# Performance work log

Measured on AMD Instinct MI355X. Metric: run time of the kernel, lower is better.

The kernel has to match this reference:

```python
import jax, jax.numpy as jnp
import numpy as np

B, S, D, H = 2, 2048, 1024, 16
HD = D // H
SCALE = HD ** -0.5

def setup_inputs() -> dict:
    key = jax.random.key(0)
    ks = jax.random.split(key, 5)
    x = jax.random.normal(ks[0], (B, S, D), dtype=jnp.float32)
    Wqkv = jax.random.normal(ks[1], (D, 3 * D), dtype=jnp.float32) * (D ** -0.5)
    bqkv = jnp.zeros((3 * D,), dtype=jnp.float32)
    Wproj = jax.random.normal(ks[2], (D, D), dtype=jnp.float32) * (D ** -0.5)
    bproj = jnp.zeros((D,), dtype=jnp.float32)
    return {"x": x, "Wqkv": Wqkv, "bqkv": bqkv, "Wproj": Wproj, "bproj": bproj}

def reference(x, Wqkv, bqkv, Wproj, bproj):
    b, s, _ = x.shape
    qkv = x @ Wqkv + bqkv                       # [B,S,3D]
    qkv = qkv.reshape(b, s, 3, H, HD)
    q, k, v = [jnp.transpose(qkv[:, :, i], (0, 2, 1, 3)) for i in range(3)]  # [B,H,S,HD]
    attn = jnp.einsum('bhqd,bhkd->bhqk', q, k) * SCALE   # [B,H,S,S]
    attn = jax.nn.softmax(attn, axis=-1)
    out = jnp.einsum('bhqk,bhkd->bhqd', attn, v)         # [B,H,S,HD]
    out = jnp.transpose(out, (0, 2, 1, 3)).reshape(b, s, D)
    return out @ Wproj + bproj
```

## Files before the change

### kernel.cpp

```cpp
#include <hip/hip_runtime.h>
#include <hip/hip_bf16.h>

#define BB 2
#define SS 2048
#define DD 1024
#define HH 16
#define HDD 64
#define MM (BB*SS)
#define NQKV (3*DD)
#define SCALE 0.125f
#define QPRESCALE 0.18033688f

typedef __bf16 bf16_t;
typedef bf16_t bf16x4 __attribute__((ext_vector_type(4)));
typedef bf16_t bf16x8 __attribute__((ext_vector_type(8)));
typedef float f32x4 __attribute__((ext_vector_type(4)));
typedef float f32x16 __attribute__((ext_vector_type(16)));

__device__ __forceinline__ void gl_lds16(const bf16_t* g, bf16_t* l) {
    __builtin_amdgcn_global_load_lds(
        (const __attribute__((address_space(1))) unsigned int*)(uintptr_t)g,
        (__attribute__((address_space(3))) unsigned int*)(uintptr_t)l,
        16, 0, 0);
}

__global__ __launch_bounds__(256) void convert_f32_bf16(
    const float* __restrict__ src, bf16_t* __restrict__ dst, int n)
{
    int i = (blockIdx.x * 256 + threadIdx.x) * 8;
    if (i < n) {
        float4 a = *(const float4*)(src + i);
        float4 b = *(const float4*)(src + i + 4);
        bf16x8 v;
        v[0]=(bf16_t)a.x; v[1]=(bf16_t)a.y; v[2]=(bf16_t)a.z; v[3]=(bf16_t)a.w;
        v[4]=(bf16_t)b.x; v[5]=(bf16_t)b.y; v[6]=(bf16_t)b.z; v[7]=(bf16_t)b.w;
        *reinterpret_cast<bf16x8*>(dst + i) = v;
    }
}

__global__ __launch_bounds__(256) void transpose2_f32_bf16(
    const float* __restrict__ Wqkv, const float* __restrict__ Wproj,
    bf16_t* __restrict__ wqkvt, bf16_t* __restrict__ wprojt)
{
    __shared__ float tile[32][33];
    const int bx = blockIdx.x;
    const float* src; bf16_t* dst; int C, bxl;
    if (bx < 96) { src = Wqkv;  dst = wqkvt;  C = NQKV; bxl = bx; }
    else         { src = Wproj; dst = wprojt; C = DD;   bxl = bx - 96; }
    const int R = DD;
    const int tx = threadIdx.x & 31, ty = threadIdx.x >> 5;
    const int r0 = blockIdx.y * 32, c0 = bxl * 32;
    #pragma unroll
    for (int i = 0; i < 32; i += 8)
        tile[ty + i][tx] = src[(size_t)(r0 + ty + i) * C + c0 + tx];
    __syncthreads();
    #pragma unroll
    for (int i = 0; i < 32; i += 8)
        dst[(size_t)(c0 + ty + i) * R + r0 + tx] = (bf16_t)tile[tx][ty + i];
}

template <int MODE>
__global__ __launch_bounds__(256) void gemm_bt(
    const bf16_t* __restrict__ A, const bf16_t* __restrict__ Bt,
    const float* __restrict__ bias, float* __restrict__ outf,
    bf16_t* __restrict__ qw, bf16_t* __restrict__ kw, bf16_t* __restrict__ vtw,
    int N, int K)
{
    __shared__ __align__(16) bf16_t As[128 * 32];
    __shared__ __align__(16) bf16_t Bs[128 * 32];

    const int tid  = threadIdx.x;
    const int w    = tid >> 6;
    const int lane = tid & 63;
    const int lr   = lane & 15;
    const int quad = lane >> 4;
    const int m0   = blockIdx.y * 128;
    const int n0   = blockIdx.x * 128;
    const int wm   = w >> 1;
    const int wn   = w & 1;

    f32x4 acc[4][4];
    #pragma unroll
    for (int i = 0; i < 4; i++)
        #pragma unroll
        for (int j = 0; j < 4; j++) acc[i][j] = (f32x4){0.f, 0.f, 0.f, 0.f};

    const int stgRow = lane >> 2;
    const int stgCol = (lane & 3) * 8;
    const bf16_t* aPtr = A  + (size_t)(m0 + w * 32 + stgRow) * K + stgCol;
    const bf16_t* bPtr = Bt + (size_t)(n0 + w * 32 + stgRow) * K + stgCol;
    bf16_t* aDst = As + w * 1024;
    bf16_t* bDst = Bs + w * 1024;
    const size_t rowSkip = (size_t)16 * K;

    for (int ks = 0; ks < K; ks += 32) {
        __syncthreads();
        gl_lds16(aPtr + ks,           aDst);
        gl_lds16(aPtr + rowSkip + ks, aDst + 512);
        gl_lds16(bPtr + ks,           bDst);
        gl_lds16(bPtr + rowSkip + ks, bDst + 512);
        __syncthreads();

        bf16x8 af[4], bf[4];
        #pragma unroll
        for (int mi = 0; mi < 4; mi++)
            af[mi] = *reinterpret_cast<const bf16x8*>(&As[(wm * 64 + mi * 16 + lr) * 32 + quad * 8]);
        #pragma unroll
        for (int ni = 0; ni < 4; ni++)
            bf[ni] = *reinterpret_cast<const bf16x8*>(&Bs[(wn * 64 + ni * 16 + lr) * 32 + quad * 8]);
        #pragma unroll
        for (int mi = 0; mi < 4; mi++)
            #pragma unroll
            for (int ni = 0; ni < 4; ni++)
                acc[mi][ni] = __builtin_amdgcn_mfma_f32_16x16x32_bf16(af[mi], bf[ni], acc[mi][ni], 0, 0, 0);
    }

    #pragma unroll
    for (int mi = 0; mi < 4; mi++) {
        #pragma unroll
        for (int ni = 0; ni < 4; ni++) {
            #pragma unroll
            for (int reg = 0; reg < 4; reg++) {
                int row = m0 + wm * 64 + mi * 16 + quad * 4 + reg;
                int col = n0 + wn * 64 + ni * 16 + lr;
                float val = acc[mi][ni][reg] + bias[col];
                if constexpr (MODE == 0) {
                    int b = row >> 11, s = row & 2047;
                    int which = col >> 10, d = col & 1023;
                    int h = d >> 6, hd = d & 63;
                    size_t bh = (size_t)(b * HH + h);
                    if (which == 0)      qw[(bh * SS + s) * HDD + hd] = (bf16_t)(val * QPRESCALE);
                    else if (which == 1) kw[(bh * SS + s) * HDD + hd] = (bf16_t)val;
                    else                 vtw[(bh * HDD + hd) * SS + s] = (bf16_t)val;
                } else {
                    outf[(size_t)row * N + col] = val;
                }
            }
        }
    }
}

__global__ __launch_bounds__(256) void gemm_bt64(
    const bf16_t* __restrict__ A, const bf16_t* __restrict__ Bt,
    const float* __restrict__ bias, float* __restrict__ outf, int N, int K)
{
    __shared__ __align__(16) bf16_t As[64 * 32];
    __shared__ __align__(16) bf16_t Bs[128 * 32];

    const int tid  = threadIdx.x;
    const int w    = tid >> 6;
    const int lane = tid & 63;
    const int lr   = lane & 15;
    const int quad = lane >> 4;
    const int m0   = blockIdx.y * 64;
    const int n0   = blockIdx.x * 128;
    const int wm   = w >> 1;
    const int wn   = w & 1;

    f32x4 acc[2][4];
    #pragma unroll
    for (int i = 0; i < 2; i++)
        #pragma unroll
        for (int j = 0; j < 4; j++) acc[i][j] = (f32x4){0.f, 0.f, 0.f, 0.f};

    const int stgRow = lane >> 2;
    const int stgCol = (lane & 3) * 8;
    const bf16_t* aPtr = A  + (size_t)(m0 + w * 16 + stgRow) * K + stgCol;
    const bf16_t* bPtr = Bt + (size_t)(n0 + w * 32 + stgRow) * K + stgCol;
    bf16_t* aDst = As + w * 512;
    bf16_t* bDst = Bs + w * 1024;
    const size_t rowSkip = (size_t)16 * K;

    for (int ks = 0; ks < K; ks += 32) {
        __syncthreads();
        gl_lds16(aPtr + ks,           aDst);
        gl_lds16(bPtr + ks,           bDst);
        gl_lds16(bPtr + rowSkip + ks, bDst + 512);
        __syncthreads();

        bf16x8 af[2], bf[4];
        #pragma unroll
        for (int mi = 0; mi < 2; mi++)
            af[mi] = *reinterpret_cast<const bf16x8*>(&As[(wm * 32 + mi * 16 + lr) * 32 + quad * 8]);
        #pragma unroll
        for (int ni = 0; ni < 4; ni++)
            bf[ni] = *reinterpret_cast<const bf16x8*>(&Bs[(wn * 64 + ni * 16 + lr) * 32 + quad * 8]);
        #pragma unroll
        for (int mi = 0; mi < 2; mi++)
            #pragma unroll
            for (int ni = 0; ni < 4; ni++)
                acc[mi][ni] = __builtin_amdgcn_mfma_f32_16x16x32_bf16(af[mi], bf[ni], acc[mi][ni], 0, 0, 0);
    }

    #pragma unroll
    for (int mi = 0; mi < 2; mi++)
        #pragma unroll
        for (int ni = 0; ni < 4; ni++)
            #pragma unroll
            for (int reg = 0; reg < 4; reg++) {
                int row = m0 + wm * 32 + mi * 16 + quad * 4 + reg;
                int col = n0 + wn * 64 + ni * 16 + lr;
                outf[(size_t)row * N + col] = acc[mi][ni][reg] + bias[col];
            }
}

__global__ __launch_bounds__(512, 4) void attn_kernel(
    const bf16_t* __restrict__ qws, const bf16_t* __restrict__ kws,
    const bf16_t* __restrict__ vtws, bf16_t* __restrict__ ob)
{
    __shared__ __align__(16) bf16_t smem[17024];
    bf16_t* Ks = smem;
    bf16_t* Vs = smem + 8320;

    const int tid  = threadIdx.x;
    const int w    = tid >> 6;
    const int g    = w >> 2;
    const int wg   = w & 3;
    const int lane = tid & 63;
    const int ln31 = lane & 31;
    const int ln5  = lane >> 5;

    const int qb = blockIdx.x;
    const int bh = blockIdx.y;
    const int b  = bh >> 4;
    const int h  = bh & 15;

    const bf16_t* Qh  = qws  + (size_t)bh * SS * HDD;
    const bf16_t* Kh  = kws  + (size_t)bh * SS * HDD;
    const bf16_t* Vth = vtws + (size_t)bh * HDD * SS;

    const int q0w    = qb * 128 + wg * 32;
    const int kvbase = g * 1024;
    const int kofs   = g * 520;
    const int vofs   = g * 4352;

    bf16x8 aq[4];
    #pragma unroll
    for (int f = 0; f < 4; f++)
        aq[f] = *(const bf16x8*)(Qh + (size_t)(q0w + ln31) * HDD + f * 16 + ln5 * 8);

    const int gtid = tid & 255;
    const int sc = gtid & 7;
    const int sr = gtid >> 3;

    {
        bf16x8 k0 = *(const bf16x8*)(Kh  + (size_t)(kvbase + sr     ) * HDD + sc * 8);
        bf16x8 k1 = *(const bf16x8*)(Kh  + (size_t)(kvbase + sr + 32) * HDD + sc * 8);
        bf16x8 v0 = *(const bf16x8*)(Vth + (size_t)(sr     ) * SS + kvbase + sc * 8);
        bf16x8 v1 = *(const bf16x8*)(Vth + (size_t)(sr + 32) * SS + kvbase + sc * 8);
        *reinterpret_cast<bf16x8*>(&Ks[(kofs + sc * 65 + sr     ) * 8]) = k0;
        *reinterpret_cast<bf16x8*>(&Ks[(kofs + sc * 65 + sr + 32) * 8]) = k1;
        bf16_t* vd0 = &Vs[vofs + (sr     ) * 68 + sc * 8];
        bf16_t* vd1 = &Vs[vofs + (sr + 32) * 68 + sc * 8];
        *reinterpret_cast<bf16x4*>(vd0)     = __builtin_shufflevector(v0, v0, 0,1,2,3);
        *reinterpret_cast<bf16x4*>(vd0 + 4) = __builtin_shufflevector(v0, v0, 4,5,6,7);
        *reinterpret_cast<bf16x4*>(vd1)     = __builtin_shufflevector(v1, v1, 0,1,2,3);
        *reinterpret_cast<bf16x4*>(vd1 + 4) = __builtin_shufflevector(v1, v1, 4,5,6,7);
    }
    __syncthreads();

    float l = 0.f;
    f32x16 o[2];
    #pragma unroll
    for (int nh = 0; nh < 2; nh++)
        #pragma unroll
        for (int r = 0; r < 16; r++) o[nh][r] = 0.f;

    for (int it = 0; it < 16; ++it) {
        f32x16 sfr[2];
        #pragma unroll
        for (int ni = 0; ni < 2; ni++) {
            #pragma unroll
            for (int r = 0; r < 16; r++) sfr[ni][r] = 0.f;
            #pragma unroll
            for (int f = 0; f < 4; f++) {
                bf16x8 kb = *reinterpret_cast<const bf16x8*>(
                    &Ks[(kofs + (2 * f + ln5) * 65 + ni * 32 + ln31) * 8]);
                sfr[ni] = __builtin_amdgcn_mfma_f32_32x32x16_bf16(kb, aq[f], sfr[ni], 0, 0, 0);
            }
        }

        bf16x8 nk0, nk1, nv0, nv1;
        const bool more = (it + 1 < 16);
        if (more) {
            const int kvn = kvbase + (it + 1) * 64;
            nk0 = *(const bf16x8*)(Kh  + (size_t)(kvn + sr     ) * HDD + sc * 8);
            nk1 = *(const bf16x8*)(Kh  + (size_t)(kvn + sr + 32) * HDD + sc * 8);
            nv0 = *(const bf16x8*)(Vth + (size_t)(sr     ) * SS + kvn + sc * 8);
            nv1 = *(const bf16x8*)(Vth + (size_t)(sr + 32) * SS + kvn + sc * 8);
        }

        float p[2][16];
        #pragma unroll
        for (int ni = 0; ni < 2; ni++)
            #pragma unroll
            for (int r = 0; r < 16; r++) {
                p[ni][r] = __builtin_amdgcn_exp2f(sfr[ni][r]);
                l += p[ni][r];
            }

        bf16x8 ap[4];
        #pragma unroll
        for (int c16 = 0; c16 < 4; c16++)
            #pragma unroll
            for (int j = 0; j < 8; j++)
                ap[c16][j] = (bf16_t)p[c16 >> 1][(c16 & 1) * 8 + j];

        #pragma unroll
        for (int nh = 0; nh < 2; nh++) {
            const bf16_t* vrow = &Vs[vofs + (nh * 32 + ln31) * 68];
            #pragma unroll
            for (int c16 = 0; c16 < 4; c16++) {
                bf16x4 lo = *(const bf16x4*)(vrow + c16 * 16 + 4 * ln5);
                bf16x4 hi = *(const bf16x4*)(vrow + c16 * 16 + 8 + 4 * ln5);
                bf16x8 vb = __builtin_shufflevector(lo, hi, 0, 1, 2, 3, 4, 5, 6, 7);
                o[nh] = __builtin_amdgcn_mfma_f32_32x32x16_bf16(ap[c16], vb, o[nh], 0, 0, 0);
            }
        }

        if (more) {
            __syncthreads();
            *reinterpret_cast<bf16x8*>(&Ks[(kofs + sc * 65 + sr     ) * 8]) = nk0;
            *reinterpret_cast<bf16x8*>(&Ks[(kofs + sc * 65 + sr + 32) * 8]) = nk1;
            bf16_t* vd0 = &Vs[vofs + (sr     ) * 68 + sc * 8];
            bf16_t* vd1 = &Vs[vofs + (sr + 32) * 68 + sc * 8];
            *reinterpret_cast<bf16x4*>(vd0)     = __builtin_shufflevector(nv0, nv0, 0,1,2,3);
            *reinterpret_cast<bf16x4*>(vd0 + 4) = __builtin_shufflevector(nv0, nv0, 4,5,6,7);
            *reinterpret_cast<bf16x4*>(vd1)     = __builtin_shufflevector(nv1, nv1, 0,1,2,3);
            *reinterpret_cast<bf16x4*>(vd1 + 4) = __builtin_shufflevector(nv1, nv1, 4,5,6,7);
            __syncthreads();
        }
    }

    l += __shfl_xor(l, 32, 64);

    __syncthreads();
    float* Of = (float*)smem;
    float* Lf = (float*)(smem + 16384);
    if (ln5 == 0) Lf[g * 128 + wg * 32 + ln31] = l;
    if (g == 1) {
        #pragma unroll
        for (int nh = 0; nh < 2; nh++)
            #pragma unroll
            for (int r = 0; r < 16; r++) {
                const int q = (r & 3) + 8 * (r >> 2) + 4 * ln5;
                Of[(wg * 32 + q) * 64 + nh * 32 + ln31] = o[nh][r];
            }
    }
    __syncthreads();
    if (g == 0) {
        float inv[16];
        #pragma unroll
        for (int r = 0; r < 16; r++) {
            const int q = (r & 3) + 8 * (r >> 2) + 4 * ln5;
            inv[r] = 1.f / (Lf[wg * 32 + q] + Lf[128 + wg * 32 + q]);
        }
        #pragma unroll
        for (int nh = 0; nh < 2; nh++)
            #pragma unroll
            for (int r = 0; r < 16; r++) {
                const int q  = (r & 3) + 8 * (r >> 2) + 4 * ln5;
                const int hd = nh * 32 + ln31;
                float val = (o[nh][r] + Of[(wg * 32 + q) * 64 + hd]) * inv[r];
                ob[((size_t)b * SS + q0w + q) * DD + h * HDD + hd] = (bf16_t)val;
            }
    }
}

extern "C" void kernel_launch(void* const* d_in, const int* in_sizes, int n_in,
                              void* d_out, int out_size, void* d_ws, size_t ws_size,
                              hipStream_t stream) {
    const float* x     = (const float*)d_in[0];
    const float* Wqkv  = (const float*)d_in[1];
    const float* bqkv  = (const float*)d_in[2];
    const float* Wproj = (const float*)d_in[3];
    const float* bproj = (const float*)d_in[4];
    float* out = (float*)d_out;

    const size_t NEL = (size_t)MM * DD;
    bf16_t* qws    = (bf16_t*)d_ws;
    bf16_t* kws    = qws  + NEL;
    bf16_t* vtws   = kws  + NEL;
    bf16_t* xb     = vtws + NEL;
    bf16_t* ows    = xb;
    bf16_t* wqkvt  = xb + NEL;
    bf16_t* wprojt = wqkvt + (size_t)NQKV * DD;

    convert_f32_bf16<<<(int)(NEL / 8 / 256), 256, 0, stream>>>(x, xb, (int)NEL);
    transpose2_f32_bf16<<<dim3(128, 32), 256, 0, stream>>>(Wqkv, Wproj, wqkvt, wprojt);

    gemm_bt<0><<<dim3(NQKV / 128, MM / 128), 256, 0, stream>>>(
        xb, wqkvt, bqkv, nullptr, qws, kws, vtws, NQKV, DD);

    attn_kernel<<<dim3(SS / 128, BB * HH), 512, 0, stream>>>(qws, kws, vtws, ows);

    gemm_bt64<<<dim3(DD / 128, MM / 64), 256, 0, stream>>>(
        ows, wprojt, bproj, out, DD, DD);
}
```

Before: 195.4 us.

## Fuse prep kernels, stage K=64 per GEMM iteration, vectorize V-transpose epilogue

Merges the x conversion and weight transpose kernels into one launch with a flattened grid, saving a launch. Both GEMMs now load two 32-wide K slices into LDS per barrier pair, halving the number of syncthreads per K and giving more loads in flight per barrier. The QKV epilogue splits by output region so V^T stores four consecutive sequence elements as one bf16x4 write instead of scattered scalar stores. LDS use doubles per block, which may reduce occupancy.

```diff
diff --git a/kernel.cpp b/kernel.cpp
--- a/kernel.cpp
+++ b/kernel.cpp
@@ -24,32 +24,36 @@
         16, 0, 0);
 }
 
-__global__ __launch_bounds__(256) void convert_f32_bf16(
-    const float* __restrict__ src, bf16_t* __restrict__ dst, int n)
+__global__ __launch_bounds__(256) void prep(
+    const float* __restrict__ x, const float* __restrict__ Wqkv,
+    const float* __restrict__ Wproj, bf16_t* __restrict__ xb,
+    bf16_t* __restrict__ wqkvt, bf16_t* __restrict__ wprojt)
 {
-    int i = (blockIdx.x * 256 + threadIdx.x) * 8;
-    if (i < n) {
-        float4 a = *(const float4*)(src + i);
-        float4 b = *(const float4*)(src + i + 4);
+    const int bx = blockIdx.x;
+    if (bx < 2048) {
+        int i = (bx * 256 + threadIdx.x) * 8;
+        float4 a = *(const float4*)(x + i);
+        float4 b = *(const float4*)(x + i + 4);
         bf16x8 v;
         v[0]=(bf16_t)a.x; v[1]=(bf16_t)a.y; v[2]=(bf16_t)a.z; v[3]=(bf16_t)a.w;
         v[4]=(bf16_t)b.x; v[5]=(bf16_t)b.y; v[6]=(bf16_t)b.z; v[7]=(bf16_t)b.w;
-        *reinterpret_cast<bf16x8*>(dst + i) = v;
-    }
-}
-
-__global__ __launch_bounds__(256) void transpose2_f32_bf16(
-    const float* __restrict__ Wqkv, const float* __restrict__ Wproj,
-    bf16_t* __restrict__ wqkvt, bf16_t* __restrict__ wprojt)
-{
+        *reinterpret_cast<bf16x8*>(xb + i) = v;
+        return;
+    }
     __shared__ float tile[32][33];
-    const int bx = blockIdx.x;
-    const float* src; bf16_t* dst; int C, bxl;
-    if (bx < 96) { src = Wqkv;  dst = wqkvt;  C = NQKV; bxl = bx; }
-    else         { src = Wproj; dst = wprojt; C = DD;   bxl = bx - 96; }
+    const float* src; bf16_t* dst; int C, bxl, byl;
+    if (bx < 5120) {
+        int t = bx - 2048;
+        byl = t / 96; bxl = t - byl * 96;
+        src = Wqkv;  dst = wqkvt;  C = NQKV;
+    } else {
+        int t = bx - 5120;
+        byl = t >> 5; bxl = t & 31;
+        src = Wproj; dst = wprojt; C = DD;
+    }
     const int R = DD;
     const int tx = threadIdx.x & 31, ty = threadIdx.x >> 5;
-    const int r0 = blockIdx.y * 32, c0 = bxl * 32;
+    const int r0 = byl * 32, c0 = bxl * 32;
     #pragma unroll
     for (int i = 0; i < 32; i += 8)
         tile[ty + i][tx] = src[(size_t)(r0 + ty + i) * C + c0 + tx];
@@ -66,8 +70,8 @@
     bf16_t* __restrict__ qw, bf16_t* __restrict__ kw, bf16_t* __restrict__ vtw,
     int N, int K)
 {
-    __shared__ __align__(16) bf16_t As[128 * 32];
-    __shared__ __align__(16) bf16_t Bs[128 * 32];
+    __shared__ __align__(16) bf16_t As[2][128 * 32];
+    __shared__ __align__(16) bf16_t Bs[2][128 * 32];
 
     const int tid  = threadIdx.x;
     const int w    = tid >> 6;
@@ -89,54 +93,90 @@
     const int stgCol = (lane & 3) * 8;
     const bf16_t* aPtr = A  + (size_t)(m0 + w * 32 + stgRow) * K + stgCol;
     const bf16_t* bPtr = Bt + (size_t)(n0 + w * 32 + stgRow) * K + stgCol;
-    bf16_t* aDst = As + w * 1024;
-    bf16_t* bDst = Bs + w * 1024;
     const size_t rowSkip = (size_t)16 * K;
 
-    for (int ks = 0; ks < K; ks += 32) {
+    for (int ks = 0; ks < K; ks += 64) {
         __syncthreads();
-        gl_lds16(aPtr + ks,           aDst);
-        gl_lds16(aPtr + rowSkip + ks, aDst + 512);
-        gl_lds16(bPtr + ks,           bDst);
-        gl_lds16(bPtr + rowSkip + ks, bDst + 512);
+        #pragma unroll
+        for (int s = 0; s < 2; s++) {
+            const int ko = ks + s * 32;
+            gl_lds16(aPtr + ko,           &As[s][w * 1024]);
+            gl_lds16(aPtr + rowSkip + ko, &As[s][w * 1024 + 512]);
+            gl_lds16(bPtr + ko,           &Bs[s][w * 1024]);
+            gl_lds16(bPtr + rowSkip + ko, &Bs[s][w * 1024 + 512]);
+        }
         __syncthreads();
 
-        bf16x8 af[4], bf[4];
+        #pragma unroll
+        for (int s = 0; s < 2; s++) {
+            bf16x8 af[4], bf[4];
+            #pragma unroll
+            for (int mi = 0; mi < 4; mi++)
+                af[mi] = *reinterpret_cast<const bf16x8*>(&As[s][(wm * 64 + mi * 16 + lr) * 32 + quad * 8]);
+            #pragma unroll
+            for (int ni = 0; ni < 4; ni++)
+                bf[ni] = *reinterpret_cast<const bf16x8*>(&Bs[s][(wn * 64 + ni * 16 + lr) * 32 + quad * 8]);
+            #pragma unroll
+            for (int mi = 0; mi < 4; mi++)
+                #pragma unroll
+                for (int ni = 0; ni < 4; ni++)
+                    acc[mi][ni] = __builtin_amdgcn_mfma_f32_16x16x32_bf16(af[mi], bf[ni], acc[mi][ni], 0, 0, 0);
+        }
+    }
+
+    if constexpr (MODE == 0) {
+        const int which = n0 >> 10;
+        if (which == 2) {
+            #pragma unroll
+            for (int mi = 0; mi < 4; mi++) {
+                #pragma unroll
+                for (int ni = 0; ni < 4; ni++) {
+                    const int row0 = m0 + wm * 64 + mi * 16 + quad * 4;
+                    const int col  = n0 + wn * 64 + ni * 16 + lr;
+                    const int b = row0 >> 11, s0 = row0 & 2047;
+                    const int d = col & 1023;
+                    const int h = d >> 6, hd = d & 63;
+                    const float bc = bias[col];
+                    bf16x4 v;
+                    v[0] = (bf16_t)(acc[mi][ni][0] + bc);
+                    v[1] = (bf16_t)(acc[mi][ni][1] + bc);
+                    v[2] = (bf16_t)(acc[mi][ni][2] + bc);
+                    v[3] = (bf16_t)(acc[mi][ni][3] + bc);
+                    *reinterpret_cast<bf16x4*>(
+                        &vtw[((size_t)(b * HH + h) * HDD + hd) * SS + s0]) = v;
+                }
+            }
+        } else {
+            bf16_t* dst = (which == 0) ? qw : kw;
+            const float mul = (which == 0) ? QPRESCALE : 1.f;
+            #pragma unroll
+            for (int mi = 0; mi < 4; mi++)
+                #pragma unroll
+                for (int ni = 0; ni < 4; ni++) {
+                    const int col = n0 + wn * 64 + ni * 16 + lr;
+                    const int d = col & 1023;
+                    const int h = d >> 6, hd = d & 63;
+                    const float bc = bias[col];
+                    #pragma unroll
+                    for (int reg = 0; reg < 4; reg++) {
+                        const int row = m0 + wm * 64 + mi * 16 + quad * 4 + reg;
+                        const int b = row >> 11, s = row & 2047;
+                        dst[((size_t)(b * HH + h) * SS + s) * HDD + hd] =
+                            (bf16_t)((acc[mi][ni][reg] + bc) * mul);
+                    }
+                }
+        }
+    } else {
         #pragma unroll
         for (int mi = 0; mi < 4; mi++)
-            af[mi] = *reinterpret_cast<const bf16x8*>(&As[(wm * 64 + mi * 16 + lr) * 32 + quad * 8]);
-        #pragma unroll
-        for (int ni = 0; ni < 4; ni++)
-            bf[ni] = *reinterpret_cast<const bf16x8*>(&Bs[(wn * 64 + ni * 16 + lr) * 32 + quad * 8]);
-        #pragma unroll
-        for (int mi = 0; mi < 4; mi++)
             #pragma unroll
             for (int ni = 0; ni < 4; ni++)
-                acc[mi][ni] = __builtin_amdgcn_mfma_f32_16x16x32_bf16(af[mi], bf[ni], acc[mi][ni], 0, 0, 0);
-    }
-
-    #pragma unroll
-    for (int mi = 0; mi < 4; mi++) {
-        #pragma unroll
-        for (int ni = 0; ni < 4; ni++) {
-            #pragma unroll
-            for (int reg = 0; reg < 4; reg++) {
-                int row = m0 + wm * 64 + mi * 16 + quad * 4 + reg;
-                int col = n0 + wn * 64 + ni * 16 + lr;
-                float val = acc[mi][ni][reg] + bias[col];
-                if constexpr (MODE == 0) {
-                    int b = row >> 11, s = row & 2047;
-                    int which = col >> 10, d = col & 1023;
-                    int h = d >> 6, hd = d & 63;
-                    size_t bh = (size_t)(b * HH + h);
-                    if (which == 0)      qw[(bh * SS + s) * HDD + hd] = (bf16_t)(val * QPRESCALE);
-                    else if (which == 1) kw[(bh * SS + s) * HDD + hd] = (bf16_t)val;
-                    else                 vtw[(bh * HDD + hd) * SS + s] = (bf16_t)val;
-                } else {
-                    outf[(size_t)row * N + col] = val;
+                #pragma unroll
+                for (int reg = 0; reg < 4; reg++) {
+                    const int row = m0 + wm * 64 + mi * 16 + quad * 4 + reg;
+                    const int col = n0 + wn * 64 + ni * 16 + lr;
+                    outf[(size_t)row * N + col] = acc[mi][ni][reg] + bias[col];
                 }
-            }
-        }
     }
 }
 
@@ -144,8 +184,8 @@
     const bf16_t* __restrict__ A, const bf16_t* __restrict__ Bt,
     const float* __restrict__ bias, float* __restrict__ outf, int N, int K)
 {
-    __shared__ __align__(16) bf16_t As[64 * 32];
-    __shared__ __align__(16) bf16_t Bs[128 * 32];
+    __shared__ __align__(16) bf16_t As[2][64 * 32];
+    __shared__ __align__(16) bf16_t Bs[2][128 * 32];
 
     const int tid  = threadIdx.x;
     const int w    = tid >> 6;
@@ -167,29 +207,34 @@
     const int stgCol = (lane & 3) * 8;
     const bf16_t* aPtr = A  + (size_t)(m0 + w * 16 + stgRow) * K + stgCol;
     const bf16_t* bPtr = Bt + (size_t)(n0 + w * 32 + stgRow) * K + stgCol;
-    bf16_t* aDst = As + w * 512;
-    bf16_t* bDst = Bs + w * 1024;
     const size_t rowSkip = (size_t)16 * K;
 
-    for (int ks = 0; ks < K; ks += 32) {
+    for (int ks = 0; ks < K; ks += 64) {
         __syncthreads();
-        gl_lds16(aPtr + ks,           aDst);
-        gl_lds16(bPtr + ks,           bDst);
-        gl_lds16(bPtr + rowSkip + ks, bDst + 512);
+        #pragma unroll
+        for (int s = 0; s < 2; s++) {
+            const int ko = ks + s * 32;
+            gl_lds16(aPtr + ko,           &As[s][w * 512]);
+            gl_lds16(bPtr + ko,           &Bs[s][w * 1024]);
+            gl_lds16(bPtr + rowSkip + ko, &Bs[s][w * 1024 + 512]);
+        }
         __syncthreads();
 
-        bf16x8 af[2], bf[4];
-        #pragma unroll
-        for (int mi = 0; mi < 2; mi++)
-            af[mi] = *reinterpret_cast<const bf16x8*>(&As[(wm * 32 + mi * 16 + lr) * 32 + quad * 8]);
-        #pragma unroll
-        for (int ni = 0; ni < 4; ni++)
-            bf[ni] = *reinterpret_cast<const bf16x8*>(&Bs[(wn * 64 + ni * 16 + lr) * 32 + quad * 8]);
-        #pragma unroll
-        for (int mi = 0; mi < 2; mi++)
+        #pragma unroll
+        for (int s = 0; s < 2; s++) {
+            bf16x8 af[2], bf[4];
+            #pragma unroll
+            for (int mi = 0; mi < 2; mi++)
+                af[mi] = *reinterpret_cast<const bf16x8*>(&As[s][(wm * 32 + mi * 16 + lr) * 32 + quad * 8]);
             #pragma unroll
             for (int ni = 0; ni < 4; ni++)
-                acc[mi][ni] = __builtin_amdgcn_mfma_f32_16x16x32_bf16(af[mi], bf[ni], acc[mi][ni], 0, 0, 0);
+                bf[ni] = *reinterpret_cast<const bf16x8*>(&Bs[s][(wn * 64 + ni * 16 + lr) * 32 + quad * 8]);
+            #pragma unroll
+            for (int mi = 0; mi < 2; mi++)
+                #pragma unroll
+                for (int ni = 0; ni < 4; ni++)
+                    acc[mi][ni] = __builtin_amdgcn_mfma_f32_16x16x32_bf16(af[mi], bf[ni], acc[mi][ni], 0, 0, 0);
+        }
     }
 
     #pragma unroll
@@ -386,8 +431,7 @@
     bf16_t* wqkvt  = xb + NEL;
     bf16_t* wprojt = wqkvt + (size_t)NQKV * DD;
 
-    convert_f32_bf16<<<(int)(NEL / 8 / 256), 256, 0, stream>>>(x, xb, (int)NEL);
-    transpose2_f32_bf16<<<dim3(128, 32), 256, 0, stream>>>(Wqkv, Wproj, wqkvt, wprojt);
+    prep<<<6144, 256, 0, stream>>>(x, Wqkv, Wproj, xb, wqkvt, wprojt);
 
     gemm_bt<0><<<dim3(NQKV / 128, MM / 128), 256, 0, stream>>>(
         xb, wqkvt, bqkv, nullptr, qws, kws, vtws, NQKV, DD);
```

Result: faster. 191.0 us (-2.3%).
